# Performance work log

Measured on AMD Instinct MI355X. Metric: run time of the kernel, lower is better.

## Reference

```python
import jax, jax.numpy as jnp
import numpy as np

N = 100000
IN_DIM, HID, OUT = 64, 128, 64
BN_EPS = 1e-5
DEG_EPS = 1e-6


def gcn_layer(x, row, col, W, b):
    # deg[i] = out-count of node i as a destination (bincount of row)
    deg = jax.ops.segment_sum(jnp.ones_like(row, dtype=x.dtype), row, num_segments=N)
    deg = deg[:, None] + DEG_EPS
    # agg[row[e]] += x[col[e]]  (gather + scatter-add)
    agg = jax.ops.segment_sum(x[col], row, num_segments=N) / deg
    return agg @ W.T + b


def batchnorm_train(x, gamma, beta):
    # training-mode BN over the node dimension (biased variance, like torch)
    mean = jnp.mean(x, axis=0)
    var = jnp.mean(jnp.square(x - mean), axis=0)
    return (x - mean) * jax.lax.rsqrt(var + BN_EPS) * gamma + beta


def setup_inputs() -> dict:
    key = jax.random.key(0)
    ks = jax.random.split(key, 8)
    x = jax.random.normal(ks[0], (N, IN_DIM), dtype=jnp.float32)
    edge_index = jax.random.randint(ks[1], (2, 1600000), 0, N, dtype=jnp.int64)

    def lin(k, out_d, in_d):
        lim = 1.0 / np.sqrt(in_d)
        kw, kb = jax.random.split(k)
        W = jax.random.uniform(kw, (out_d, in_d), jnp.float32, -lim, lim)
        b = jax.random.uniform(kb, (out_d,), jnp.float32, -lim, lim)
        return W, b

    W1, b1 = lin(ks[2], HID, IN_DIM)
    W2, b2 = lin(ks[3], HID, HID)
    W3, b3 = lin(ks[4], OUT, HID)
    return {
        "x": x, "edge_index": edge_index,
        "W1": W1, "b1": b1,
        "gamma1": jnp.ones((HID,), jnp.float32), "beta1": jnp.zeros((HID,), jnp.float32),
        "W2": W2, "b2": b2,
        "gamma2": jnp.ones((HID,), jnp.float32), "beta2": jnp.zeros((HID,), jnp.float32),
        "W3": W3, "b3": b3,
    }


def reference(x, edge_index, W1, b1, gamma1, beta1, W2, b2, gamma2, beta2, W3, b3):
    row, col = edge_index[0], edge_index[1]
    h = gcn_layer(x, row, col, W1, b1)
    h = jax.nn.relu(batchnorm_train(h, gamma1, beta1))  # dropout: eval/identity
    h = gcn_layer(h, row, col, W2, b2)
    h = jax.nn.relu(batchnorm_train(h, gamma2, beta2))
    return gcn_layer(h, row, col, W3, b3)
```

## Files before the change

### kernel.cpp

```cpp
#include <hip/hip_runtime.h>
#include <hip/hip_bf16.h>


using short8 = __attribute__((ext_vector_type(8))) short;
using f32x4  = __attribute__((ext_vector_type(4))) float;
using f32x2  = __attribute__((ext_vector_type(2))) float;

__device__ __forceinline__ float bf_lo(unsigned int u) { return __uint_as_float(u << 16); }
__device__ __forceinline__ float bf_hi(unsigned int u) { return __uint_as_float(u & 0xffff0000u); }
__device__ __forceinline__ f32x2 bfpair(unsigned int u) {
    f32x2 r;
    r.x = __uint_as_float(u << 16);
    r.y = __uint_as_float(u & 0xffff0000u);
    return r;
}
__device__ __forceinline__ unsigned short f2bf(float f) {
    __hip_bfloat16 h = __float2bfloat16(f);
    return *reinterpret_cast<unsigned short*>(&h);
}
__device__ __forceinline__ int clampi(int v, int lo, int hi) {
    return v < lo ? lo : (v > hi ? hi : v);
}

#define BSH 7
#define CHUNK 2048


struct CvtPack {
    const void* src[10];
    void* dstA[10];
    void* dstB[10];
    int sz[10];
    int mode[10];
};

__global__ void cvt_params_kernel(CvtPack pp, const unsigned int* __restrict__ gamma_raw,
                                  const int* __restrict__ edge_raw, int* __restrict__ flags) {
    int bf = (gamma_raw[0] == 0x3F803F80u) ? 1 : 0;
    if (blockIdx.x == 0 && threadIdx.x == 0) {
        flags[0] = bf;
        int is64 = 1;
        for (int i = 1; i <= 15; i += 2)
            if (edge_raw[i] != 0) is64 = 0;
        flags[1] = is64;
    }
    int b = blockIdx.x;
    int sz = pp.sz[b];
    for (int i = threadIdx.x; i < sz; i += blockDim.x) {
        float w = bf ? __bfloat162float(((const __hip_bfloat16*)pp.src[b])[i])
                     : ((const float*)pp.src[b])[i];
        if (pp.mode[b] == 0) {
            ((float*)pp.dstA[b])[i] = w;
        } else {
            __hip_bfloat16 hi = __float2bfloat16(w);
            float r = w - __bfloat162float(hi);
            ((__hip_bfloat16*)pp.dstA[b])[i] = hi;
            ((__hip_bfloat16*)pp.dstB[b])[i] = __float2bfloat16(r);
        }
    }
}

__global__ __launch_bounds__(256) void xcvt_kernel(const float* __restrict__ x,
                                                   const unsigned int* __restrict__ gamma_raw,
                                                   __hip_bfloat16* __restrict__ xbf,
                                                   int total8) {
    if (gamma_raw[0] == 0x3F803F80u) return;
    int idx = blockIdx.x * 256 + threadIdx.x;
    int stride = gridDim.x * 256;
    for (; idx < total8; idx += stride) {
        const float* p = x + (size_t)idx * 8;
        float4 a = *reinterpret_cast<const float4*>(p);
        float4 b = *reinterpret_cast<const float4*>(p + 4);
        uint4 o;
        o.x = ((unsigned)f2bf(a.y) << 16) | f2bf(a.x);
        o.y = ((unsigned)f2bf(a.w) << 16) | f2bf(a.z);
        o.z = ((unsigned)f2bf(b.y) << 16) | f2bf(b.x);
        o.w = ((unsigned)f2bf(b.w) << 16) | f2bf(b.z);
        *reinterpret_cast<uint4*>(xbf + (size_t)idx * 8) = o;
    }
}


__global__ __launch_bounds__(256) void bucket_count_kernel(
    const int* __restrict__ edge, const int* __restrict__ flags,
    int* __restrict__ bucket_cnt, int E, int n, int NB) {
    __shared__ int hist[1024];
    for (int i = threadIdx.x; i < NB; i += 256) hist[i] = 0;
    __syncthreads();
    int base = blockIdx.x * CHUNK;
    int end = base + CHUNK < E ? base + CHUNK : E;
    int is64 = flags[1];
    for (int e = base + (int)threadIdx.x; e < end; e += 256) {
        int r = is64 ? edge[2 * e] : edge[e];
        r = clampi(r, 0, n - 1);
        atomicAdd(&hist[r >> BSH], 1);
    }
    __syncthreads();
    for (int i = threadIdx.x; i < NB; i += 256) {
        int v = hist[i];
        if (v) atomicAdd(&bucket_cnt[i], v);
    }
}

__global__ __launch_bounds__(1024) void bucket_scan_kernel(
    const int* __restrict__ bucket_cnt, int* __restrict__ bucket_base,
    int* __restrict__ bucket_cursor, int* __restrict__ row_ptr, int NB, int n, int E) {
    __shared__ int sh[1024];
    int t = threadIdx.x;
    int v = (t < NB) ? bucket_cnt[t] : 0;
    sh[t] = v;
    __syncthreads();
    for (int off = 1; off < 1024; off <<= 1) {
        int u = (t >= off) ? sh[t - off] : 0;
        __syncthreads();
        sh[t] += u;
        __syncthreads();
    }
    if (t < NB) {
        int base = sh[t] - v;
        bucket_base[t] = base;
        bucket_cursor[t] = base;
    }
    if (t == 0) row_ptr[n] = E;
}

__global__ __launch_bounds__(256) void bucket_scatter_kernel(
    const int* __restrict__ edge, const int* __restrict__ flags,
    int* __restrict__ bucket_cursor, unsigned* __restrict__ packed,
    int E, int n, int NB) {
    __shared__ int hist[1024];
    __shared__ int cur[1024];
    int t = threadIdx.x;
    for (int i = t; i < NB; i += 256) hist[i] = 0;
    __syncthreads();
    int base = blockIdx.x * CHUNK;
    int end = base + CHUNK < E ? base + CHUNK : E;
    int is64 = flags[1];
    for (int e = base + t; e < end; e += 256) {
        int r = is64 ? edge[2 * e] : edge[e];
        r = clampi(r, 0, n - 1);
        atomicAdd(&hist[r >> BSH], 1);
    }
    __syncthreads();
    for (int i = t; i < NB; i += 256) {
        int h = hist[i];
        cur[i] = h ? atomicAdd(&bucket_cursor[i], h) : 0;
    }
    __syncthreads();
    for (int e = base + t; e < end; e += 256) {
        int r = is64 ? edge[2 * e] : edge[e];
        int c = is64 ? edge[2 * (E + e)] : edge[E + e];
        r = clampi(r, 0, n - 1);
        c = clampi(c, 0, n - 1);
        int p = atomicAdd(&cur[r >> BSH], 1);
        packed[p] = ((unsigned)(r & 127) << 17) | (unsigned)c;
    }
}

#define SORT_CAP 4096
__global__ __launch_bounds__(256) void bucket_sort_kernel(
    const unsigned* __restrict__ packed, const int* __restrict__ bucket_base,
    const int* __restrict__ bucket_cnt, int* __restrict__ row_ptr,
    int* __restrict__ col_sorted, int n) {
    __shared__ int hist[128], cur[128];
    __shared__ int out[SORT_CAP];
    int b = blockIdx.x;
    int s = bucket_base[b];
    int cnt = bucket_cnt[b];
    int t = threadIdx.x;
    if (t < 128) hist[t] = 0;
    __syncthreads();
    for (int i = t; i < cnt; i += 256) atomicAdd(&hist[packed[s + i] >> 17], 1);
    __syncthreads();
    int orig = (t < 128) ? hist[t] : 0;
    for (int off = 1; off < 128; off <<= 1) {
        int u = (t < 128 && t >= off) ? hist[t - off] : 0;
        __syncthreads();
        if (t < 128) hist[t] += u;
        __syncthreads();
    }
    if (t < 128) {
        int ex = hist[t] - orig;
        cur[t] = ex;
        int node = (b << BSH) + t;
        if (node < n) row_ptr[node] = s + ex;
    }
    __syncthreads();
    if (cnt <= SORT_CAP) {
        for (int i = t; i < cnt; i += 256) {
            unsigned pk = packed[s + i];
            int p = atomicAdd(&cur[pk >> 17], 1);
            out[p] = (int)(pk & 0x1FFFFu);
        }
        __syncthreads();
        for (int i = t; i < cnt; i += 256) col_sorted[s + i] = out[i];
    } else {
        for (int i = t; i < cnt; i += 256) {
            unsigned pk = packed[s + i];
            int p = atomicAdd(&cur[pk >> 17], 1);
            col_sorted[s + p] = (int)(pk & 0x1FFFFu);
        }
    }
}


__device__ __forceinline__ void accum_u4(uint4 u, f32x2* acc) {
    acc[0] += bfpair(u.x);
    acc[1] += bfpair(u.y);
    acc[2] += bfpair(u.z);
    acc[3] += bfpair(u.w);
}

template <int D>
__device__ __forceinline__ void gather_bf(const __hip_bfloat16* __restrict__ base,
                                          const int* __restrict__ cols,
                                          int s, int e, int sub, f32x2* acc) {
    constexpr int LPR = D / 8;
    constexpr int EPW = 64 / LPR;
    int cnt = e - s;
    int nfull = cnt / EPW;
    int rem = cnt - nfull * EPW;
    int k = s + sub;
    int it = 0;
    for (; it + 4 <= nfull; it += 4) {
        int c0 = cols[k];
        int c1 = cols[k + EPW];
        int c2 = cols[k + 2 * EPW];
        int c3 = cols[k + 3 * EPW];
        uint4 u0 = *reinterpret_cast<const uint4*>(base + (size_t)c0 * D);
        uint4 u1 = *reinterpret_cast<const uint4*>(base + (size_t)c1 * D);
        uint4 u2 = *reinterpret_cast<const uint4*>(base + (size_t)c2 * D);
        uint4 u3 = *reinterpret_cast<const uint4*>(base + (size_t)c3 * D);
        accum_u4(u0, acc);
        accum_u4(u1, acc);
        accum_u4(u2, acc);
        accum_u4(u3, acc);
        k += 4 * EPW;
    }
    if (it + 2 <= nfull) {
        int c0 = cols[k];
        int c1 = cols[k + EPW];
        uint4 u0 = *reinterpret_cast<const uint4*>(base + (size_t)c0 * D);
        uint4 u1 = *reinterpret_cast<const uint4*>(base + (size_t)c1 * D);
        accum_u4(u0, acc);
        accum_u4(u1, acc);
        k += 2 * EPW;
        it += 2;
    }
    if (it < nfull) {
        uint4 u = *reinterpret_cast<const uint4*>(base + (size_t)cols[k] * D);
        accum_u4(u, acc);
    }
    if (sub < rem) {
        uint4 u = *reinterpret_cast<const uint4*>(
            base + (size_t)cols[s + nfull * EPW + sub] * D);
        accum_u4(u, acc);
    }
}

template <int D, bool ADD_BIAS, bool OUT_FLAGDT>
__global__ __launch_bounds__(256) void agg_vec_kernel(
    const __hip_bfloat16* __restrict__ src, const int* __restrict__ row_ptr,
    const int* __restrict__ col_sorted, const float* __restrict__ bias,
    void* __restrict__ outp, const int* __restrict__ flags, int n) {
    constexpr int LPR = D / 8;
    int lane = threadIdx.x & 63;
    int node = blockIdx.x * 4 + (threadIdx.x >> 6);
    if (node >= n) return;
    int sub = lane / LPR;
    int c0 = (lane % LPR) * 8;

    int s = row_ptr[node];
    int e = row_ptr[node + 1];
    f32x2 acc[4];
#pragma unroll
    for (int j = 0; j < 4; ++j) acc[j] = (f32x2){0.f, 0.f};

    gather_bf<D>(src + c0, col_sorted, s, e, sub, acc);

#pragma unroll
    for (int j = 0; j < 4; ++j)
#pragma unroll
        for (int off = LPR; off < 64; off <<= 1) {
            acc[j].x += __shfl_xor(acc[j].x, off, 64);
            acc[j].y += __shfl_xor(acc[j].y, off, 64);
        }

    if (lane < LPR) {
        float recip = 1.0f / ((float)(e - s) + 1e-6f);
        float m[8];
#pragma unroll
        for (int j = 0; j < 4; ++j) {
            m[2 * j] = acc[j].x * recip;
            m[2 * j + 1] = acc[j].y * recip;
        }
        if (ADD_BIAS) {
#pragma unroll
            for (int j = 0; j < 8; ++j) m[j] += bias[c0 + j];
        }
        bool as_bf = !OUT_FLAGDT || flags[0];
        if (as_bf) {
            uint4 o;
            o.x = ((unsigned)f2bf(m[1]) << 16) | f2bf(m[0]);
            o.y = ((unsigned)f2bf(m[3]) << 16) | f2bf(m[2]);
            o.z = ((unsigned)f2bf(m[5]) << 16) | f2bf(m[4]);
            o.w = ((unsigned)f2bf(m[7]) << 16) | f2bf(m[6]);
            *reinterpret_cast<uint4*>((__hip_bfloat16*)outp + (size_t)node * D + c0) = o;
        } else {
            float* op = (float*)outp + (size_t)node * D + c0;
            *reinterpret_cast<float4*>(op) = make_float4(m[0], m[1], m[2], m[3]);
            *reinterpret_cast<float4*>(op + 4) = make_float4(m[4], m[5], m[6], m[7]);
        }
    }
}

__global__ __launch_bounds__(256) void agg_x_kernel(
    const void* __restrict__ xsrc, const __hip_bfloat16* __restrict__ xbf,
    const int* __restrict__ flags,
    const int* __restrict__ row_ptr, const int* __restrict__ col_sorted,
    __hip_bfloat16* __restrict__ out, int n) {
    constexpr int D = 64, LPR = 8;
    int lane = threadIdx.x & 63;
    int node = blockIdx.x * 4 + (threadIdx.x >> 6);
    if (node >= n) return;
    int sub = lane / LPR;
    int c0 = (lane % LPR) * 8;
    int s = row_ptr[node];
    int e = row_ptr[node + 1];
    f32x2 acc[4];
#pragma unroll
    for (int j = 0; j < 4; ++j) acc[j] = (f32x2){0.f, 0.f};

    const __hip_bfloat16* src = flags[0] ? (const __hip_bfloat16*)xsrc : xbf;
    gather_bf<D>(src + c0, col_sorted, s, e, sub, acc);

#pragma unroll
    for (int j = 0; j < 4; ++j)
#pragma unroll
        for (int off = LPR; off < 64; off <<= 1) {
            acc[j].x += __shfl_xor(acc[j].x, off, 64);
            acc[j].y += __shfl_xor(acc[j].y, off, 64);
        }

    if (lane < LPR) {
        float recip = 1.0f / ((float)(e - s) + 1e-6f);
        float m[8];
#pragma unroll
        for (int j = 0; j < 4; ++j) {
            m[2 * j] = acc[j].x * recip;
            m[2 * j + 1] = acc[j].y * recip;
        }
        uint4 o;
        o.x = ((unsigned)f2bf(m[1]) << 16) | f2bf(m[0]);
        o.y = ((unsigned)f2bf(m[3]) << 16) | f2bf(m[2]);
        o.z = ((unsigned)f2bf(m[5]) << 16) | f2bf(m[4]);
        o.w = ((unsigned)f2bf(m[7]) << 16) | f2bf(m[6]);
        *reinterpret_cast<uint4*>(out + (size_t)node * D + c0) = o;
    }
}


template <int D, int F, bool BIAS, bool APPLY_BN_A, bool STATS>
__global__ __launch_bounds__(256) void gemm_mfma_kernel(
    const __hip_bfloat16* __restrict__ A, const __hip_bfloat16* __restrict__ Whi,
    const __hip_bfloat16* __restrict__ Wlo, const float* __restrict__ bias,
    const float* __restrict__ bn_sums_in, const float* __restrict__ gamma,
    const float* __restrict__ beta, float inv_n,
    float* __restrict__ stats, __hip_bfloat16* __restrict__ C, int n) {
    constexpr int JT = F / 16;
    constexpr int KCH = D / 32;
    constexpr int NF = KCH * JT * 2;
    __shared__ uint4 wlds[NF * 64];
    __shared__ float ssl[256];

    int t = threadIdx.x;
    if (APPLY_BN_A && t < 128) {
        float mean = bn_sums_in[t] * inv_n;
        float var = bn_sums_in[128 + t] * inv_n - mean * mean;
        float inv = rsqrtf(var + 1e-5f);
        float sc = gamma[t] * inv;
        ssl[t] = sc;
        ssl[128 + t] = beta[t] - mean * sc;
    }
    for (int idx = t; idx < NF * 64; idx += 256) {
        int f = idx >> 6, ln = idx & 63;
        int kc = f / (JT * 2);
        int rem = f % (JT * 2);
        int jt = rem >> 1, h = rem & 1;
        int mm = ln & 15, qq = ln >> 4;
        const __hip_bfloat16* src =
            (h ? Wlo : Whi) + (size_t)(jt * 16 + mm) * D + kc * 32 + qq * 8;
        wlds[idx] = *reinterpret_cast<const uint4*>(src);
    }
    if (APPLY_BN_A) __syncthreads();

    int lane = t & 63;
    int wave = t >> 6;
    int m = lane & 15;
    int quad = lane >> 4;
    int row_base = blockIdx.x * 128 + wave * 32;

    short8 af[2][KCH];
#pragma unroll
    for (int rs = 0; rs < 2; ++rs) {
        int r = row_base + rs * 16 + m;
        r = r < n ? r : n - 1;
        const __hip_bfloat16* ap = A + (size_t)r * D + quad * 8;
#pragma unroll
        for (int kc = 0; kc < KCH; ++kc) {
            union { uint4 u; short8 s; } tmp;
            tmp.u = *reinterpret_cast<const uint4*>(ap + kc * 32);
            af[rs][kc] = tmp.s;
        }
    }
    if (APPLY_BN_A) {
#pragma unroll
        for (int kc = 0; kc < KCH; ++kc) {
            int ch0 = kc * 32 + quad * 8;
            float sc[8], sh[8];
            *reinterpret_cast<float4*>(sc) = *reinterpret_cast<const float4*>(ssl + ch0);
            *reinterpret_cast<float4*>(sc + 4) = *reinterpret_cast<const float4*>(ssl + ch0 + 4);
            *reinterpret_cast<float4*>(sh) = *reinterpret_cast<const float4*>(ssl + 128 + ch0);
            *reinterpret_cast<float4*>(sh + 4) = *reinterpret_cast<const float4*>(ssl + 128 + ch0 + 4);
#pragma unroll
            for (int rs = 0; rs < 2; ++rs) {
#pragma unroll
                for (int j = 0; j < 8; ++j) {
                    float v = __uint_as_float(
                        ((unsigned)(unsigned short)af[rs][kc][j]) << 16);
                    v = fmaxf(fmaf(v, sc[j], sh[j]), 0.f);
                    af[rs][kc][j] = (short)f2bf(v);
                }
            }
        }
    }

    f32x4 acc[2][JT];
#pragma unroll
    for (int rs = 0; rs < 2; ++rs)
#pragma unroll
        for (int j = 0; j < JT; ++j) acc[rs][j] = {0.f, 0.f, 0.f, 0.f};

    if (!APPLY_BN_A) __syncthreads();

#pragma unroll
    for (int kc = 0; kc < KCH; ++kc) {
#pragma unroll
        for (int jt = 0; jt < JT; ++jt) {
            int fb = (kc * JT + jt) * 2;
            union { uint4 u; short8 s; } bh, bl;
            bh.u = wlds[fb * 64 + lane];
            bl.u = wlds[(fb + 1) * 64 + lane];
            acc[0][jt] = __builtin_amdgcn_mfma_f32_16x16x32_bf16(af[0][kc], bh.s, acc[0][jt], 0, 0, 0);
            acc[1][jt] = __builtin_amdgcn_mfma_f32_16x16x32_bf16(af[1][kc], bh.s, acc[1][jt], 0, 0, 0);
            acc[0][jt] = __builtin_amdgcn_mfma_f32_16x16x32_bf16(af[0][kc], bl.s, acc[0][jt], 0, 0, 0);
            acc[1][jt] = __builtin_amdgcn_mfma_f32_16x16x32_bf16(af[1][kc], bl.s, acc[1][jt], 0, 0, 0);
        }
    }

#pragma unroll
    for (int rs = 0; rs < 2; ++rs) {
#pragma unroll
        for (int jt = 0; jt < JT; ++jt) {
            int col = jt * 16 + m;
            float bv = BIAS ? bias[col] : 0.f;
#pragma unroll
            for (int i = 0; i < 4; ++i) {
                int row = row_base + rs * 16 + quad * 4 + i;
                if (row < n)
                    C[(size_t)row * F + col] = __float2bfloat16(acc[rs][jt][i] + bv);
            }
        }
    }

    if (STATS) {
        float* slds = reinterpret_cast<float*>(wlds);
        __syncthreads();
        for (int i = t; i < 2 * F; i += 256) slds[i] = 0.f;
        __syncthreads();
#pragma unroll
        for (int jt = 0; jt < JT; ++jt) {
            int col = jt * 16 + m;
            float bv = BIAS ? bias[col] : 0.f;
            float s = 0.f, q = 0.f;
#pragma unroll
            for (int rs = 0; rs < 2; ++rs) {
#pragma unroll
                for (int i = 0; i < 4; ++i) {
                    int row = row_base + rs * 16 + quad * 4 + i;
                    if (row < n) {
                        float v = acc[rs][jt][i] + bv;
                        s += v;
                        q += v * v;
                    }
                }
            }
            s += __shfl_xor(s, 16, 64); s += __shfl_xor(s, 32, 64);
            q += __shfl_xor(q, 16, 64); q += __shfl_xor(q, 32, 64);
            if (quad == 0) {
                atomicAdd(&slds[col], s);
                atomicAdd(&slds[F + col], q);
            }
        }
        __syncthreads();
        for (int i = t; i < 2 * F; i += 256) atomicAdd(&stats[i], slds[i]);
    }
}


__global__ __launch_bounds__(256) void bn_apply_kernel(__hip_bfloat16* __restrict__ X,
                                                       int ngroups,
                                                       const float* __restrict__ sums,
                                                       const float* __restrict__ gamma,
                                                       const float* __restrict__ beta,
                                                       float inv_n) {
    __shared__ float lss[256];
    int t = threadIdx.x;
    if (t < 128) {
        float mean = sums[t] * inv_n;
        float var = sums[128 + t] * inv_n - mean * mean;
        float inv = rsqrtf(var + 1e-5f);
        float sc = gamma[t] * inv;
        lss[t] = sc;
        lss[128 + t] = beta[t] - mean * sc;
    }
    __syncthreads();
    int idx = blockIdx.x * 256 + t;
    int stride = gridDim.x * 256;
    for (; idx < ngroups; idx += stride) {
        int c0 = (idx & 15) * 8;
        uint4 u = *reinterpret_cast<uint4*>(X + (size_t)idx * 8);
        float v[8];
        v[0] = bf_lo(u.x); v[1] = bf_hi(u.x);
        v[2] = bf_lo(u.y); v[3] = bf_hi(u.y);
        v[4] = bf_lo(u.z); v[5] = bf_hi(u.z);
        v[6] = bf_lo(u.w); v[7] = bf_hi(u.w);
#pragma unroll
        for (int j = 0; j < 8; ++j) {
            float tv = fmaf(v[j], lss[c0 + j], lss[128 + c0 + j]);
            v[j] = tv > 0.f ? tv : 0.f;
        }
        uint4 o;
        o.x = ((unsigned)f2bf(v[1]) << 16) | f2bf(v[0]);
        o.y = ((unsigned)f2bf(v[3]) << 16) | f2bf(v[2]);
        o.z = ((unsigned)f2bf(v[5]) << 16) | f2bf(v[4]);
        o.w = ((unsigned)f2bf(v[7]) << 16) | f2bf(v[6]);
        *reinterpret_cast<uint4*>(X + (size_t)idx * 8) = o;
    }
}


extern "C" void kernel_launch(void* const* d_in, const int* in_sizes, int n_in,
                              void* d_out, int out_size, void* d_ws, size_t ws_size,
                              hipStream_t stream) {
    const void* x   = d_in[0];
    const int* edge = (const int*)d_in[1];

    int n = in_sizes[0] / 64;
    int E = in_sizes[1] / 2;
    int NB = (n + 127) >> BSH;
    float inv_n = 1.0f / (float)n;

    char* p = (char*)d_ws;
    auto carve = [&](size_t bytes) {
        char* q = p;
        p += (bytes + 255) & ~(size_t)255;
        return q;
    };
    int* flags      = (int*)carve(64);
    float* params   = (float*)carve(1024 * 4);
    __hip_bfloat16* Whi1 = (__hip_bfloat16*)carve(8192 * 2);
    __hip_bfloat16* Wlo1 = (__hip_bfloat16*)carve(8192 * 2);
    __hip_bfloat16* Whi2 = (__hip_bfloat16*)carve(16384 * 2);
    __hip_bfloat16* Wlo2 = (__hip_bfloat16*)carve(16384 * 2);
    __hip_bfloat16* Whi3 = (__hip_bfloat16*)carve(8192 * 2);
    __hip_bfloat16* Wlo3 = (__hip_bfloat16*)carve(8192 * 2);
    int* row_ptr    = (int*)carve((size_t)(n + 1) * 4);
    int* bucket_cnt = (int*)carve(1024 * 4);
    int* bucket_base= (int*)carve(1024 * 4);
    int* bucket_cur = (int*)carve(1024 * 4);
    float* bn_sums  = (float*)carve(512 * 4);
    unsigned* packed= (unsigned*)carve((size_t)E * 4);
    int* col_sorted = (int*)carve((size_t)E * 4);
    __hip_bfloat16* xbf  = (__hip_bfloat16*)carve((size_t)n * 64 * 2);
    __hip_bfloat16* bufA = (__hip_bfloat16*)carve((size_t)n * 128 * 2);
    __hip_bfloat16* bufB = (__hip_bfloat16*)carve((size_t)n * 128 * 2);
    carve(65536);

    float* b1f = params;
    float* g1f = b1f + 128;
    float* be1f = g1f + 128;
    float* b2f = be1f + 128;
    float* g2f = b2f + 128;
    float* be2f = g2f + 128;
    float* b3f = be2f + 128;

    xcvt_kernel<<<2048, 256, 0, stream>>>((const float*)x, (const unsigned int*)d_in[4],
                                          xbf, n * 8);

    CvtPack pp;
    const int pidx[10] = {2, 3, 4, 5, 6, 7, 8, 9, 10, 11};
    void* pa[10] = {Whi1, b1f, g1f, be1f, Whi2, b2f, g2f, be2f, Whi3, b3f};
    void* pb[10] = {Wlo1, nullptr, nullptr, nullptr, Wlo2, nullptr, nullptr, nullptr, Wlo3, nullptr};
    const int psz[10] = {8192, 128, 128, 128, 16384, 128, 128, 128, 8192, 64};
    const int pmode[10] = {1, 0, 0, 0, 1, 0, 0, 0, 1, 0};
    for (int i = 0; i < 10; ++i) {
        pp.src[i] = d_in[pidx[i]];
        pp.dstA[i] = pa[i];
        pp.dstB[i] = pb[i];
        pp.sz[i] = psz[i];
        pp.mode[i] = pmode[i];
    }
    cvt_params_kernel<<<10, 256, 0, stream>>>(pp, (const unsigned int*)d_in[4], edge, flags);

    hipMemsetAsync(bucket_cnt, 0, 1024 * 4, stream);
    hipMemsetAsync(bn_sums, 0, 512 * 4, stream);
    int nchunks = (E + CHUNK - 1) / CHUNK;
    bucket_count_kernel<<<nchunks, 256, 0, stream>>>(edge, flags, bucket_cnt, E, n, NB);
    bucket_scan_kernel<<<1, 1024, 0, stream>>>(bucket_cnt, bucket_base, bucket_cur, row_ptr, NB, n, E);
    bucket_scatter_kernel<<<nchunks, 256, 0, stream>>>(edge, flags, bucket_cur, packed, E, n, NB);
    bucket_sort_kernel<<<NB, 256, 0, stream>>>(packed, bucket_base, bucket_cnt, row_ptr, col_sorted, n);

    int gemm_grid = (n + 127) / 128;
    int agg_grid = (n + 3) / 4;

    agg_x_kernel<<<agg_grid, 256, 0, stream>>>(x, xbf, flags, row_ptr, col_sorted, bufA, n);
    gemm_mfma_kernel<64, 128, true, false, true><<<gemm_grid, 256, 0, stream>>>(
        bufA, Whi1, Wlo1, b1f, nullptr, nullptr, nullptr, 0.f, bn_sums, bufB, n);
    bn_apply_kernel<<<1024, 256, 0, stream>>>(bufB, n * 16, bn_sums, g1f, be1f, inv_n);

    agg_vec_kernel<128, false, false><<<agg_grid, 256, 0, stream>>>(
        bufB, row_ptr, col_sorted, nullptr, bufA, flags, n);
    gemm_mfma_kernel<128, 128, true, false, true><<<gemm_grid, 256, 0, stream>>>(
        bufA, Whi2, Wlo2, b2f, nullptr, nullptr, nullptr, 0.f, bn_sums + 256, bufB, n);

    gemm_mfma_kernel<128, 64, false, true, false><<<gemm_grid, 256, 0, stream>>>(
        bufB, Whi3, Wlo3, nullptr, bn_sums + 256, g2f, be2f, inv_n, nullptr, bufA, n);
    agg_vec_kernel<64, true, true><<<agg_grid, 256, 0, stream>>>(
        bufA, row_ptr, col_sorted, b3f, d_out, flags, n);
}
```

Baseline: 441.4 us.

## Fuse BN+ReLU into second aggregation gather, merge conversion kernels and memsets

Removes the standalone batchnorm-apply pass over the hidden activations. Each gathered neighbour value now gets the BN scale/shift and ReLU applied inside the layer-2 aggregation. The parameter and x conversion kernels are merged into one launch, and the two memsets are combined by placing bn_sums next to bucket_cnt. The edge bucketing chunk size is also raised. The fusion trades one full read-write pass for extra FMA and max work per gathered edge (about 16 per node on average), and the larger chunks mean fewer blocks in the count and scatter kernels.

```diff
diff --git a/kernel.cpp b/kernel.cpp
--- a/kernel.cpp
+++ b/kernel.cpp
@@ -23,7 +23,7 @@
 }
 
 #define BSH 7
-#define CHUNK 2048
+#define CHUNK 8192
 
 
 struct CvtPack {
@@ -34,48 +34,48 @@
     int mode[10];
 };
 
-__global__ void cvt_params_kernel(CvtPack pp, const unsigned int* __restrict__ gamma_raw,
-                                  const int* __restrict__ edge_raw, int* __restrict__ flags) {
+__global__ __launch_bounds__(256) void cvt_all_kernel(
+    CvtPack pp, const unsigned int* __restrict__ gamma_raw,
+    const int* __restrict__ edge_raw, int* __restrict__ flags,
+    const float* __restrict__ x, __hip_bfloat16* __restrict__ xbf,
+    int total8, int nxblocks) {
     int bf = (gamma_raw[0] == 0x3F803F80u) ? 1 : 0;
-    if (blockIdx.x == 0 && threadIdx.x == 0) {
+    int b = blockIdx.x;
+    if (b == 0 && threadIdx.x == 0) {
         flags[0] = bf;
         int is64 = 1;
         for (int i = 1; i <= 15; i += 2)
             if (edge_raw[i] != 0) is64 = 0;
         flags[1] = is64;
     }
-    int b = blockIdx.x;
-    int sz = pp.sz[b];
-    for (int i = threadIdx.x; i < sz; i += blockDim.x) {
-        float w = bf ? __bfloat162float(((const __hip_bfloat16*)pp.src[b])[i])
-                     : ((const float*)pp.src[b])[i];
-        if (pp.mode[b] == 0) {
-            ((float*)pp.dstA[b])[i] = w;
-        } else {
-            __hip_bfloat16 hi = __float2bfloat16(w);
-            float r = w - __bfloat162float(hi);
-            ((__hip_bfloat16*)pp.dstA[b])[i] = hi;
-            ((__hip_bfloat16*)pp.dstB[b])[i] = __float2bfloat16(r);
-        }
-    }
-}
-
-__global__ __launch_bounds__(256) void xcvt_kernel(const float* __restrict__ x,
-                                                   const unsigned int* __restrict__ gamma_raw,
-                                                   __hip_bfloat16* __restrict__ xbf,
-                                                   int total8) {
-    if (gamma_raw[0] == 0x3F803F80u) return;
-    int idx = blockIdx.x * 256 + threadIdx.x;
-    int stride = gridDim.x * 256;
+    if (b < 10) {
+        int sz = pp.sz[b];
+        for (int i = threadIdx.x; i < sz; i += blockDim.x) {
+            float w = bf ? __bfloat162float(((const __hip_bfloat16*)pp.src[b])[i])
+                         : ((const float*)pp.src[b])[i];
+            if (pp.mode[b] == 0) {
+                ((float*)pp.dstA[b])[i] = w;
+            } else {
+                __hip_bfloat16 hi = __float2bfloat16(w);
+                float r = w - __bfloat162float(hi);
+                ((__hip_bfloat16*)pp.dstA[b])[i] = hi;
+                ((__hip_bfloat16*)pp.dstB[b])[i] = __float2bfloat16(r);
+            }
+        }
+        return;
+    }
+    if (bf) return;
+    int idx = (b - 10) * 256 + threadIdx.x;
+    int stride = nxblocks * 256;
     for (; idx < total8; idx += stride) {
         const float* p = x + (size_t)idx * 8;
         float4 a = *reinterpret_cast<const float4*>(p);
-        float4 b = *reinterpret_cast<const float4*>(p + 4);
+        float4 c = *reinterpret_cast<const float4*>(p + 4);
         uint4 o;
         o.x = ((unsigned)f2bf(a.y) << 16) | f2bf(a.x);
         o.y = ((unsigned)f2bf(a.w) << 16) | f2bf(a.z);
-        o.z = ((unsigned)f2bf(b.y) << 16) | f2bf(b.x);
-        o.w = ((unsigned)f2bf(b.w) << 16) | f2bf(b.z);
+        o.z = ((unsigned)f2bf(c.y) << 16) | f2bf(c.x);
+        o.w = ((unsigned)f2bf(c.w) << 16) | f2bf(c.z);
         *reinterpret_cast<uint4*>(xbf + (size_t)idx * 8) = o;
     }
 }
@@ -204,17 +204,36 @@
 }
 
 
-__device__ __forceinline__ void accum_u4(uint4 u, f32x2* acc) {
-    acc[0] += bfpair(u.x);
-    acc[1] += bfpair(u.y);
-    acc[2] += bfpair(u.z);
-    acc[3] += bfpair(u.w);
-}
-
-template <int D>
+template <bool BN>
+__device__ __forceinline__ void accum_u4_t(uint4 u, f32x2* acc,
+                                           const float* sc, const float* sh) {
+    if (!BN) {
+        acc[0] += bfpair(u.x);
+        acc[1] += bfpair(u.y);
+        acc[2] += bfpair(u.z);
+        acc[3] += bfpair(u.w);
+    } else {
+        f32x2 p;
+        p = bfpair(u.x);
+        acc[0].x += fmaxf(fmaf(p.x, sc[0], sh[0]), 0.f);
+        acc[0].y += fmaxf(fmaf(p.y, sc[1], sh[1]), 0.f);
+        p = bfpair(u.y);
+        acc[1].x += fmaxf(fmaf(p.x, sc[2], sh[2]), 0.f);
+        acc[1].y += fmaxf(fmaf(p.y, sc[3], sh[3]), 0.f);
+        p = bfpair(u.z);
+        acc[2].x += fmaxf(fmaf(p.x, sc[4], sh[4]), 0.f);
+        acc[2].y += fmaxf(fmaf(p.y, sc[5], sh[5]), 0.f);
+        p = bfpair(u.w);
+        acc[3].x += fmaxf(fmaf(p.x, sc[6], sh[6]), 0.f);
+        acc[3].y += fmaxf(fmaf(p.y, sc[7], sh[7]), 0.f);
+    }
+}
+
+template <int D, bool BN>
 __device__ __forceinline__ void gather_bf(const __hip_bfloat16* __restrict__ base,
                                           const int* __restrict__ cols,
-                                          int s, int e, int sub, f32x2* acc) {
+                                          int s, int e, int sub, f32x2* acc,
+                                          const float* sc, const float* sh) {
     constexpr int LPR = D / 8;
     constexpr int EPW = 64 / LPR;
     int cnt = e - s;
@@ -231,10 +250,10 @@
         uint4 u1 = *reinterpret_cast<const uint4*>(base + (size_t)c1 * D);
         uint4 u2 = *reinterpret_cast<const uint4*>(base + (size_t)c2 * D);
         uint4 u3 = *reinterpret_cast<const uint4*>(base + (size_t)c3 * D);
-        accum_u4(u0, acc);
-        accum_u4(u1, acc);
-        accum_u4(u2, acc);
-        accum_u4(u3, acc);
+        accum_u4_t<BN>(u0, acc, sc, sh);
+        accum_u4_t<BN>(u1, acc, sc, sh);
+        accum_u4_t<BN>(u2, acc, sc, sh);
+        accum_u4_t<BN>(u3, acc, sc, sh);
         k += 4 * EPW;
     }
     if (it + 2 <= nfull) {
@@ -242,27 +261,29 @@
         int c1 = cols[k + EPW];
         uint4 u0 = *reinterpret_cast<const uint4*>(base + (size_t)c0 * D);
         uint4 u1 = *reinterpret_cast<const uint4*>(base + (size_t)c1 * D);
-        accum_u4(u0, acc);
-        accum_u4(u1, acc);
+        accum_u4_t<BN>(u0, acc, sc, sh);
+        accum_u4_t<BN>(u1, acc, sc, sh);
         k += 2 * EPW;
         it += 2;
     }
     if (it < nfull) {
         uint4 u = *reinterpret_cast<const uint4*>(base + (size_t)cols[k] * D);
-        accum_u4(u, acc);
+        accum_u4_t<BN>(u, acc, sc, sh);
     }
     if (sub < rem) {
         uint4 u = *reinterpret_cast<const uint4*>(
             base + (size_t)cols[s + nfull * EPW + sub] * D);
-        accum_u4(u, acc);
-    }
-}
-
-template <int D, bool ADD_BIAS, bool OUT_FLAGDT>
+        accum_u4_t<BN>(u, acc, sc, sh);
+    }
+}
+
+template <int D, bool ADD_BIAS, bool OUT_FLAGDT, bool BN_SRC>
 __global__ __launch_bounds__(256) void agg_vec_kernel(
     const __hip_bfloat16* __restrict__ src, const int* __restrict__ row_ptr,
     const int* __restrict__ col_sorted, const float* __restrict__ bias,
-    void* __restrict__ outp, const int* __restrict__ flags, int n) {
+    void* __restrict__ outp, const int* __restrict__ flags, int n,
+    const float* __restrict__ sums, const float* __restrict__ gamma,
+    const float* __restrict__ beta, float inv_n) {
     constexpr int LPR = D / 8;
     int lane = threadIdx.x & 63;
     int node = blockIdx.x * 4 + (threadIdx.x >> 6);
@@ -270,13 +291,25 @@
     int sub = lane / LPR;
     int c0 = (lane % LPR) * 8;
 
+    float sc[8], sh[8];
+    if (BN_SRC) {
+#pragma unroll
+        for (int j = 0; j < 8; ++j) {
+            float mean = sums[c0 + j] * inv_n;
+            float var = sums[D + c0 + j] * inv_n - mean * mean;
+            float iv = rsqrtf(var + 1e-5f);
+            sc[j] = gamma[c0 + j] * iv;
+            sh[j] = beta[c0 + j] - mean * sc[j];
+        }
+    }
+
     int s = row_ptr[node];
     int e = row_ptr[node + 1];
     f32x2 acc[4];
 #pragma unroll
     for (int j = 0; j < 4; ++j) acc[j] = (f32x2){0.f, 0.f};
 
-    gather_bf<D>(src + c0, col_sorted, s, e, sub, acc);
+    gather_bf<D, BN_SRC>(src + c0, col_sorted, s, e, sub, acc, sc, sh);
 
 #pragma unroll
     for (int j = 0; j < 4; ++j)
@@ -332,7 +365,7 @@
     for (int j = 0; j < 4; ++j) acc[j] = (f32x2){0.f, 0.f};
 
     const __hip_bfloat16* src = flags[0] ? (const __hip_bfloat16*)xsrc : xbf;
-    gather_bf<D>(src + c0, col_sorted, s, e, sub, acc);
+    gather_bf<D, false>(src + c0, col_sorted, s, e, sub, acc, nullptr, nullptr);
 
 #pragma unroll
     for (int j = 0; j < 4; ++j)
@@ -504,48 +537,6 @@
         }
         __syncthreads();
         for (int i = t; i < 2 * F; i += 256) atomicAdd(&stats[i], slds[i]);
-    }
-}
-
-
-__global__ __launch_bounds__(256) void bn_apply_kernel(__hip_bfloat16* __restrict__ X,
-                                                       int ngroups,
-                                                       const float* __restrict__ sums,
-                                                       const float* __restrict__ gamma,
-                                                       const float* __restrict__ beta,
-                                                       float inv_n) {
-    __shared__ float lss[256];
-    int t = threadIdx.x;
-    if (t < 128) {
-        float mean = sums[t] * inv_n;
-        float var = sums[128 + t] * inv_n - mean * mean;
-        float inv = rsqrtf(var + 1e-5f);
-        float sc = gamma[t] * inv;
-        lss[t] = sc;
-        lss[128 + t] = beta[t] - mean * sc;
-    }
-    __syncthreads();
-    int idx = blockIdx.x * 256 + t;
-    int stride = gridDim.x * 256;
-    for (; idx < ngroups; idx += stride) {
-        int c0 = (idx & 15) * 8;
-        uint4 u = *reinterpret_cast<uint4*>(X + (size_t)idx * 8);
-        float v[8];
-        v[0] = bf_lo(u.x); v[1] = bf_hi(u.x);
-        v[2] = bf_lo(u.y); v[3] = bf_hi(u.y);
-        v[4] = bf_lo(u.z); v[5] = bf_hi(u.z);
-        v[6] = bf_lo(u.w); v[7] = bf_hi(u.w);
-#pragma unroll
-        for (int j = 0; j < 8; ++j) {
-            float tv = fmaf(v[j], lss[c0 + j], lss[128 + c0 + j]);
-            v[j] = tv > 0.f ? tv : 0.f;
-        }
-        uint4 o;
-        o.x = ((unsigned)f2bf(v[1]) << 16) | f2bf(v[0]);
-        o.y = ((unsigned)f2bf(v[3]) << 16) | f2bf(v[2]);
-        o.z = ((unsigned)f2bf(v[5]) << 16) | f2bf(v[4]);
-        o.w = ((unsigned)f2bf(v[7]) << 16) | f2bf(v[6]);
-        *reinterpret_cast<uint4*>(X + (size_t)idx * 8) = o;
     }
 }
 
@@ -577,9 +568,9 @@
     __hip_bfloat16* Wlo3 = (__hip_bfloat16*)carve(8192 * 2);
     int* row_ptr    = (int*)carve((size_t)(n + 1) * 4);
     int* bucket_cnt = (int*)carve(1024 * 4);
+    float* bn_sums  = (float*)carve(512 * 4);
     int* bucket_base= (int*)carve(1024 * 4);
     int* bucket_cur = (int*)carve(1024 * 4);
-    float* bn_sums  = (float*)carve(512 * 4);
     unsigned* packed= (unsigned*)carve((size_t)E * 4);
     int* col_sorted = (int*)carve((size_t)E * 4);
     __hip_bfloat16* xbf  = (__hip_bfloat16*)carve((size_t)n * 64 * 2);
@@ -594,9 +585,6 @@
     float* g2f = b2f + 128;
     float* be2f = g2f + 128;
     float* b3f = be2f + 128;
-
-    xcvt_kernel<<<2048, 256, 0, stream>>>((const float*)x, (const unsigned int*)d_in[4],
-                                          xbf, n * 8);
 
     CvtPack pp;
     const int pidx[10] = {2, 3, 4, 5, 6, 7, 8, 9, 10, 11};
@@ -611,10 +599,12 @@
         pp.sz[i] = psz[i];
         pp.mode[i] = pmode[i];
     }
-    cvt_params_kernel<<<10, 256, 0, stream>>>(pp, (const unsigned int*)d_in[4], edge, flags);
-
-    hipMemsetAsync(bucket_cnt, 0, 1024 * 4, stream);
-    hipMemsetAsync(bn_sums, 0, 512 * 4, stream);
+    const int NXB = 1024;
+    cvt_all_kernel<<<10 + NXB, 256, 0, stream>>>(
+        pp, (const unsigned int*)d_in[4], edge, flags,
+        (const float*)x, xbf, n * 8, NXB);
+
+    hipMemsetAsync(bucket_cnt, 0, 4096 + 2048, stream);
     int nchunks = (E + CHUNK - 1) / CHUNK;
     bucket_count_kernel<<<nchunks, 256, 0, stream>>>(edge, flags, bucket_cnt, E, n, NB);
     bucket_scan_kernel<<<1, 1024, 0, stream>>>(bucket_cnt, bucket_base, bucket_cur, row_ptr, NB, n, E);
@@ -627,15 +617,16 @@
     agg_x_kernel<<<agg_grid, 256, 0, stream>>>(x, xbf, flags, row_ptr, col_sorted, bufA, n);
     gemm_mfma_kernel<64, 128, true, false, true><<<gemm_grid, 256, 0, stream>>>(
         bufA, Whi1, Wlo1, b1f, nullptr, nullptr, nullptr, 0.f, bn_sums, bufB, n);
-    bn_apply_kernel<<<1024, 256, 0, stream>>>(bufB, n * 16, bn_sums, g1f, be1f, inv_n);
-
-    agg_vec_kernel<128, false, false><<<agg_grid, 256, 0, stream>>>(
-        bufB, row_ptr, col_sorted, nullptr, bufA, flags, n);
+
+    agg_vec_kernel<128, false, false, true><<<agg_grid, 256, 0, stream>>>(
+        bufB, row_ptr, col_sorted, nullptr, bufA, flags, n,
+        bn_sums, g1f, be1f, inv_n);
     gemm_mfma_kernel<128, 128, true, false, true><<<gemm_grid, 256, 0, stream>>>(
         bufA, Whi2, Wlo2, b2f, nullptr, nullptr, nullptr, 0.f, bn_sums + 256, bufB, n);
 
     gemm_mfma_kernel<128, 64, false, true, false><<<gemm_grid, 256, 0, stream>>>(
         bufB, Whi3, Wlo3, nullptr, bn_sums + 256, g2f, be2f, inv_n, nullptr, bufA, n);
-    agg_vec_kernel<64, true, true><<<agg_grid, 256, 0, stream>>>(
-        bufA, row_ptr, col_sorted, b3f, d_out, flags, n);
-}
+    agg_vec_kernel<64, true, true, false><<<agg_grid, 256, 0, stream>>>(
+        bufA, row_ptr, col_sorted, b3f, d_out, flags, n,
+        nullptr, nullptr, nullptr, 0.f);
+}
```

After: 428.3 us. 3.0% less time.
